# Optimization experiments

Hardware: AMD Instinct MI355X
Metric: run time of the kernel (lower is better)

Reference implementation:

```python
import jax, jax.numpy as jnp
import numpy as np

T, B, P, Q, WW, WF, C = 7, 512, 200, 64, 64, 256, 10
N = B * P
SIGMA = 0.1


def _lin(key, fin, fout):
    kw, kb = jax.random.split(key)
    s = 1.0 / np.sqrt(fin)
    return (jax.random.uniform(kw, (fin, fout), minval=-s, maxval=s),
            jax.random.uniform(kb, (fout,), minval=-s, maxval=s))


def setup_inputs() -> dict:
    key = jax.random.key(0)
    ks = jax.random.split(key, 9)
    diagms = jax.random.normal(ks[0], (T, N, 2), dtype=jnp.float32)
    # repeat_interleave(arange(B), counts): equal-sized segments of P points
    seg_ids = jnp.tile(jnp.repeat(jnp.arange(B, dtype=jnp.int32), P), (T, 1))
    theta = jax.random.normal(ks[1], (Q, 2), dtype=jnp.float32)
    w1, b1 = _lin(ks[2], 2, WW)
    w2, b2 = _lin(ks[3], WW, WW)
    w3, b3 = _lin(ks[4], WW, 1)
    r1, rb1 = _lin(ks[5], T * Q, WF)
    r2, rb2 = _lin(ks[6], WF, WF)
    r3, rb3 = _lin(ks[7], WF, C)
    return dict(diagms=diagms, seg_ids=seg_ids, theta=theta,
                w1=w1, b1=b1, w2=w2, b2=b2, w3=w3, b3=b3,
                r1=r1, rb1=rb1, r2=r2, rb2=rb2, r3=r3, rb3=rb3)


def reference(diagms, seg_ids, theta, w1, b1, w2, b2, w3, b3,
              r1, rb1, r2, rb2, r3, rb3):
    # gaussian kernel: exp(-||x - theta||^2 / (2 sigma^2)), cdist expanded
    diff = diagms[:, :, None, :] - theta[None, None, :, :]      # [T,N,Q,2]
    rep = jnp.exp(-jnp.sum(diff * diff, axis=-1) / (2.0 * SIGMA ** 2))  # [T,N,Q]
    # weight MLP on raw (birth,death) coords, shared across types
    h = jax.nn.relu(diagms @ w1 + b1)
    h = jax.nn.relu(h @ w2 + b2)
    w = jax.nn.sigmoid(h @ w3 + b3)                              # [T,N,1]
    rep = w * rep
    # global_mean_pool per diagram type via segment sum
    def pool(r, s):
        sums = jax.ops.segment_sum(r, s, num_segments=B)         # [B,Q]
        cnts = jax.ops.segment_sum(jnp.ones((r.shape[0],), r.dtype), s,
                                   num_segments=B)
        return sums / jnp.maximum(cnts, 1.0)[:, None]
    pooled = jax.vmap(pool)(rep, seg_ids)                        # [T,B,Q]
    topo = jnp.transpose(pooled, (1, 0, 2)).reshape(B, T * Q)    # cat over types
    # final MLP rho
    z = jax.nn.relu(topo @ r1 + rb1)
    z = jax.nn.relu(z @ r2 + rb2)
    return z @ r3 + rb3                                          # [B,C]
```

## Files before the change

### kernel.cpp

```cpp
#include <hip/hip_runtime.h>
#include <hip/hip_bf16.h>
#include <math.h>

#define TT 7
#define BB 512
#define PP 200
#define QQ 64
#define WWH 64
#define WF 256
#define CC 10
#define NN (BB * PP)
#define TQ (TT * QQ)

typedef __attribute__((ext_vector_type(8))) short short8;
typedef __attribute__((ext_vector_type(4))) float f32x4;

static __device__ __forceinline__ unsigned short f2bf(float f) {
    __hip_bfloat16 b = __float2bfloat16(f);
    return *reinterpret_cast<unsigned short*>(&b);
}

__global__ __launch_bounds__(256, 4) void point_weight_kernel(
    const float* __restrict__ diagms,
    const float* __restrict__ w1,
    const float* __restrict__ b1,
    const float* __restrict__ w2,
    const float* __restrict__ b2,
    const float* __restrict__ w3,
    const float* __restrict__ b3,
    float* __restrict__ w_out)
{
    __shared__ unsigned short Hl[256 * 64];
    __shared__ unsigned short W2T[64 * 64];

    const int tid  = threadIdx.x;
    const int lane = tid & 63;
    const int wv   = tid >> 6;

    {
        const int n  = tid & 63;
        const int j0 = (tid >> 6) * 16;
#pragma unroll
        for (int jj = 0; jj < 16; ++jj) {
            const int j = j0 + jj;
            const float v = w2[j * WWH + n];
            const int off = n * 64 + ((((j >> 3) ^ (n & 7))) << 3) + (j & 7);
            W2T[off] = f2bf(v);
        }
    }

    {
        const int p = tid;
        const float2 d = reinterpret_cast<const float2*>(diagms)[(size_t)blockIdx.x * 256 + p];
        const float x = d.x, y = d.y;
        uint4* Hrow = reinterpret_cast<uint4*>(Hl);
#pragma unroll
        for (int i = 0; i < 8; ++i) {
            unsigned int pk[4];
#pragma unroll
            for (int e = 0; e < 4; ++e) {
                const int j = i * 8 + 2 * e;
                const float h0 = fmaxf(fmaf(x, w1[j],     fmaf(y, w1[WWH + j],     b1[j])),     0.0f);
                const float h1 = fmaxf(fmaf(x, w1[j + 1], fmaf(y, w1[WWH + j + 1], b1[j + 1])), 0.0f);
                pk[e] = (unsigned int)f2bf(h0) | ((unsigned int)f2bf(h1) << 16);
            }
            uint4 v; v.x = pk[0]; v.y = pk[1]; v.z = pk[2]; v.w = pk[3];
            Hrow[p * 8 + (i ^ (p & 7))] = v;
        }
    }

    __syncthreads();

    float b2v[4], w3v[4];
#pragma unroll
    for (int nt = 0; nt < 4; ++nt) {
        b2v[nt] = b2[nt * 16 + (lane & 15)];
        w3v[nt] = w3[nt * 16 + (lane & 15)];
    }
    const float b3s = b3[0];

    short8 bf[2][4];
#pragma unroll
    for (int s = 0; s < 2; ++s) {
#pragma unroll
        for (int nt = 0; nt < 4; ++nt) {
            const int n = nt * 16 + (lane & 15);
            const int slot = ((lane >> 4) + s * 4) ^ (lane & 7);
            bf[s][nt] = reinterpret_cast<const short8*>(W2T)[n * 8 + slot];
        }
    }

    const int wave_p0 = wv * 64;
    const size_t out_base = (size_t)blockIdx.x * 256;

#pragma unroll 1
    for (int m = 0; m < 4; ++m) {
        f32x4 acc[4];
#pragma unroll
        for (int nt = 0; nt < 4; ++nt) acc[nt] = (f32x4){0.f, 0.f, 0.f, 0.f};

#pragma unroll
        for (int s = 0; s < 2; ++s) {
            const int p = wave_p0 + m * 16 + (lane & 15);
            const int slot = ((lane >> 4) + s * 4) ^ (lane & 7);
            const short8 af = reinterpret_cast<const short8*>(Hl)[p * 8 + slot];
#pragma unroll
            for (int nt = 0; nt < 4; ++nt) {
                acc[nt] = __builtin_amdgcn_mfma_f32_16x16x32_bf16(af, bf[s][nt], acc[nt], 0, 0, 0);
            }
        }

        float sum0 = 0.f, sum1 = 0.f, sum2 = 0.f, sum3 = 0.f;
#pragma unroll
        for (int nt = 0; nt < 4; ++nt) {
            sum0 = fmaf(fmaxf(acc[nt][0] + b2v[nt], 0.f), w3v[nt], sum0);
            sum1 = fmaf(fmaxf(acc[nt][1] + b2v[nt], 0.f), w3v[nt], sum1);
            sum2 = fmaf(fmaxf(acc[nt][2] + b2v[nt], 0.f), w3v[nt], sum2);
            sum3 = fmaf(fmaxf(acc[nt][3] + b2v[nt], 0.f), w3v[nt], sum3);
        }
#pragma unroll
        for (int off = 1; off < 16; off <<= 1) {
            sum0 += __shfl_xor(sum0, off, 64);
            sum1 += __shfl_xor(sum1, off, 64);
            sum2 += __shfl_xor(sum2, off, 64);
            sum3 += __shfl_xor(sum3, off, 64);
        }
        const int r_sel = lane & 15;
        if (r_sel < 4) {
            const float sv = (r_sel == 0) ? sum0 : (r_sel == 1) ? sum1
                           : (r_sel == 2) ? sum2 : sum3;
            const float wa = sv + b3s;
            const float wsig = 1.0f / (1.0f + __expf(-wa));
            const int prow = wave_p0 + m * 16 + ((lane >> 4) << 2) + r_sel;
            w_out[out_base + prow] = wsig;
        }
    }
}

#define NEG50_OVER_LN2 (-72.13475204444817f)

__global__ __launch_bounds__(256) void rep_pool_kernel(
    const float* __restrict__ diagms,
    const float* __restrict__ theta,
    const float* __restrict__ w_in,
    float* __restrict__ pooled)
{
    const int bid = blockIdx.x;
    const int t = bid >> 9;
    const int b = bid & (BB - 1);
    const int tid = threadIdx.x;

    __shared__ float px[PP];
    __shared__ float py[PP];
    __shared__ float wv[PP];

    if (tid < PP) {
        const int n = t * NN + b * PP + tid;
        const float2 d = reinterpret_cast<const float2*>(diagms)[n];
        px[tid] = d.x;
        py[tid] = d.y;
        wv[tid] = w_in[n];
    }
    __syncthreads();

    const int q = tid & (QQ - 1);
    const int g = tid >> 6;
    const float2 th = reinterpret_cast<const float2*>(theta)[q];
    const float tx = th.x;
    const float ty = th.y;

    float acc = 0.0f;
    const int p0 = g * (PP / 4);
#pragma unroll 5
    for (int p = p0; p < p0 + PP / 4; ++p) {
        const float dx = px[p] - tx;
        const float dy = py[p] - ty;
        acc = fmaf(wv[p], exp2f(fmaf(dx, dx, dy * dy) * NEG50_OVER_LN2), acc);
    }

    __shared__ float part[4][QQ];
    part[g][q] = acc;
    __syncthreads();

    if (tid < QQ) {
        const float s = (part[0][tid] + part[1][tid]) + (part[2][tid] + part[3][tid]);
        pooled[b * TQ + t * QQ + tid] = s * (1.0f / (float)PP);
    }
}

#define K3_ROWS 2
__global__ __launch_bounds__(256, 2) void rho_kernel(
    const float* __restrict__ pooled,
    const float* __restrict__ r1,
    const float* __restrict__ rb1,
    const float* __restrict__ r2,
    const float* __restrict__ rb2,
    const float* __restrict__ r3,
    const float* __restrict__ rb3,
    float* __restrict__ out)
{
    const int b0 = blockIdx.x * K3_ROWS;
    const int tid = threadIdx.x;

    __shared__ float tp[K3_ROWS * TQ];
    __shared__ float z1[K3_ROWS][WF];
    __shared__ float z2[K3_ROWS][WF];
    __shared__ float red[4][K3_ROWS][CC];

    {
        const float* src = pooled + (size_t)b0 * TQ;
#pragma unroll
        for (int j = 0; j < K3_ROWS * TQ; j += 256) {
            const int idx = j + tid;
            if (idx < K3_ROWS * TQ) tp[idx] = src[idx];
        }
    }
    __syncthreads();

    {
        float acc0 = rb1[tid], acc1 = rb1[tid];
        const float* r1c = r1 + tid;
        float rv0[8], rv1[8];
#pragma unroll
        for (int e = 0; e < 8; ++e) rv0[e] = r1c[e * WF];
#pragma unroll 1
        for (int i0 = 0; i0 < TQ; i0 += 16) {
#pragma unroll
            for (int e = 0; e < 8; ++e) rv1[e] = r1c[(i0 + 8 + e) * WF];
#pragma unroll
            for (int e = 0; e < 8; ++e) {
                acc0 = fmaf(tp[i0 + e],      rv0[e], acc0);
                acc1 = fmaf(tp[TQ + i0 + e], rv0[e], acc1);
            }
            if (i0 + 16 < TQ) {
#pragma unroll
                for (int e = 0; e < 8; ++e) rv0[e] = r1c[(i0 + 16 + e) * WF];
            }
#pragma unroll
            for (int e = 0; e < 8; ++e) {
                acc0 = fmaf(tp[i0 + 8 + e],      rv1[e], acc0);
                acc1 = fmaf(tp[TQ + i0 + 8 + e], rv1[e], acc1);
            }
        }
        z1[0][tid] = fmaxf(acc0, 0.0f);
        z1[1][tid] = fmaxf(acc1, 0.0f);
    }
    __syncthreads();

    {
        float acc0 = rb2[tid], acc1 = rb2[tid];
        const float* r2c = r2 + tid;
        float rv0[8], rv1[8];
#pragma unroll
        for (int e = 0; e < 8; ++e) rv0[e] = r2c[e * WF];
#pragma unroll 1
        for (int i0 = 0; i0 < WF; i0 += 16) {
#pragma unroll
            for (int e = 0; e < 8; ++e) rv1[e] = r2c[(i0 + 8 + e) * WF];
#pragma unroll
            for (int e = 0; e < 8; ++e) {
                acc0 = fmaf(z1[0][i0 + e], rv0[e], acc0);
                acc1 = fmaf(z1[1][i0 + e], rv0[e], acc1);
            }
            if (i0 + 16 < WF) {
#pragma unroll
                for (int e = 0; e < 8; ++e) rv0[e] = r2c[(i0 + 16 + e) * WF];
            }
#pragma unroll
            for (int e = 0; e < 8; ++e) {
                acc0 = fmaf(z1[0][i0 + 8 + e], rv1[e], acc0);
                acc1 = fmaf(z1[1][i0 + 8 + e], rv1[e], acc1);
            }
        }
        z2[0][tid] = fmaxf(acc0, 0.0f);
        z2[1][tid] = fmaxf(acc1, 0.0f);
    }
    __syncthreads();

    {
        const int lane = tid & 63;
        const int wvi  = tid >> 6;
        const float za = z2[0][tid];
        const float zb = z2[1][tid];
        float p0[CC], p1[CC];
#pragma unroll
        for (int c = 0; c < CC; ++c) {
            const float rc = r3[tid * CC + c];
            p0[c] = za * rc;
            p1[c] = zb * rc;
        }
#pragma unroll
        for (int off = 32; off >= 1; off >>= 1) {
#pragma unroll
            for (int c = 0; c < CC; ++c) {
                p0[c] += __shfl_xor(p0[c], off, 64);
                p1[c] += __shfl_xor(p1[c], off, 64);
            }
        }
        if (lane == 0) {
#pragma unroll
            for (int c = 0; c < CC; ++c) {
                red[wvi][0][c] = p0[c];
                red[wvi][1][c] = p1[c];
            }
        }
        __syncthreads();
        if (tid < K3_ROWS * CC) {
            const int r = tid / CC;
            const int c = tid % CC;
            out[(size_t)(b0 + r) * CC + c] =
                red[0][r][c] + red[1][r][c] + red[2][r][c] + red[3][r][c] + rb3[c];
        }
    }
}

extern "C" void kernel_launch(void* const* d_in, const int* in_sizes, int n_in,
                              void* d_out, int out_size, void* d_ws, size_t ws_size,
                              hipStream_t stream)
{
    const float* diagms = (const float*)d_in[0];
    const float* theta  = (const float*)d_in[2];
    const float* w1     = (const float*)d_in[3];
    const float* b1     = (const float*)d_in[4];
    const float* w2     = (const float*)d_in[5];
    const float* b2     = (const float*)d_in[6];
    const float* w3     = (const float*)d_in[7];
    const float* b3     = (const float*)d_in[8];
    const float* r1     = (const float*)d_in[9];
    const float* rb1    = (const float*)d_in[10];
    const float* r2     = (const float*)d_in[11];
    const float* rb2    = (const float*)d_in[12];
    const float* r3     = (const float*)d_in[13];
    const float* rb3    = (const float*)d_in[14];
    float* out = (float*)d_out;

    float* w_buf  = (float*)d_ws;
    float* pooled = w_buf + (size_t)TT * NN;

    const int total = TT * NN;

    point_weight_kernel<<<total / 256, 256, 0, stream>>>(
        diagms, w1, b1, w2, b2, w3, b3, w_buf);

    rep_pool_kernel<<<TT * BB, 256, 0, stream>>>(diagms, theta, w_buf, pooled);

    rho_kernel<<<BB / K3_ROWS, 256, 0, stream>>>(pooled, r1, rb1, r2, rb2, r3, rb3, out);
}
```

Measured before the change: 145.4 us.

## Fuse point-weight MLP into pooling kernel and split rho K-dimension across waves

Merges the per-point weight MLP kernel with the Gaussian representation pooling kernel. Each block of one diagram now computes weights for 256 loaded points, of which 200 are used, and keeps them in shared memory. This removes the global write and re-read of the weight buffer and one kernel launch, at the cost of about 28% redundant MLP work on padding points. The rho kernel now uses 1024 threads, splitting each layer's reduction dimension into four slices with a shared-memory partial sum. This adds parallelism and latency hiding to the small final MLP.

```diff
diff --git a/kernel.cpp b/kernel.cpp
--- a/kernel.cpp
+++ b/kernel.cpp
@@ -20,22 +20,32 @@
     return *reinterpret_cast<unsigned short*>(&b);
 }
 
-__global__ __launch_bounds__(256, 4) void point_weight_kernel(
+#define NEG50_OVER_LN2 (-72.13475204444817f)
+
+__global__ __launch_bounds__(256, 3) void fused_weight_pool_kernel(
     const float* __restrict__ diagms,
+    const float* __restrict__ theta,
     const float* __restrict__ w1,
     const float* __restrict__ b1,
     const float* __restrict__ w2,
     const float* __restrict__ b2,
     const float* __restrict__ w3,
     const float* __restrict__ b3,
-    float* __restrict__ w_out)
+    float* __restrict__ pooled)
 {
     __shared__ unsigned short Hl[256 * 64];
     __shared__ unsigned short W2T[64 * 64];
-
+    __shared__ float px[256];
+    __shared__ float py[256];
+    __shared__ float wv[256];
+    __shared__ float part[4][QQ];
+
+    const int bid  = blockIdx.x;
+    const int t    = bid >> 9;
+    const int b    = bid & (BB - 1);
     const int tid  = threadIdx.x;
     const int lane = tid & 63;
-    const int wv   = tid >> 6;
+    const int wvx  = tid >> 6;
 
     {
         const int n  = tid & 63;
@@ -50,9 +60,13 @@
     }
 
     {
-        const int p = tid;
-        const float2 d = reinterpret_cast<const float2*>(diagms)[(size_t)blockIdx.x * 256 + p];
+        const int base = t * NN + b * PP;
+        int gidx = base + tid;
+        if (gidx > TT * NN - 1) gidx = TT * NN - 1;
+        const float2 d = reinterpret_cast<const float2*>(diagms)[gidx];
         const float x = d.x, y = d.y;
+        px[tid] = x;
+        py[tid] = y;
         uint4* Hrow = reinterpret_cast<uint4*>(Hl);
 #pragma unroll
         for (int i = 0; i < 8; ++i) {
@@ -65,121 +79,96 @@
                 pk[e] = (unsigned int)f2bf(h0) | ((unsigned int)f2bf(h1) << 16);
             }
             uint4 v; v.x = pk[0]; v.y = pk[1]; v.z = pk[2]; v.w = pk[3];
-            Hrow[p * 8 + (i ^ (p & 7))] = v;
-        }
-    }
-
-    __syncthreads();
-
-    float b2v[4], w3v[4];
-#pragma unroll
-    for (int nt = 0; nt < 4; ++nt) {
-        b2v[nt] = b2[nt * 16 + (lane & 15)];
-        w3v[nt] = w3[nt * 16 + (lane & 15)];
-    }
-    const float b3s = b3[0];
-
-    short8 bf[2][4];
-#pragma unroll
-    for (int s = 0; s < 2; ++s) {
+            Hrow[tid * 8 + (i ^ (tid & 7))] = v;
+        }
+    }
+
+    __syncthreads();
+
+    {
+        float b2v[4], w3v[4];
 #pragma unroll
         for (int nt = 0; nt < 4; ++nt) {
-            const int n = nt * 16 + (lane & 15);
-            const int slot = ((lane >> 4) + s * 4) ^ (lane & 7);
-            bf[s][nt] = reinterpret_cast<const short8*>(W2T)[n * 8 + slot];
-        }
-    }
-
-    const int wave_p0 = wv * 64;
-    const size_t out_base = (size_t)blockIdx.x * 256;
+            b2v[nt] = b2[nt * 16 + (lane & 15)];
+            w3v[nt] = w3[nt * 16 + (lane & 15)];
+        }
+        const float b3s = b3[0];
+
+        short8 bfr[2][4];
+#pragma unroll
+        for (int s = 0; s < 2; ++s) {
+#pragma unroll
+            for (int nt = 0; nt < 4; ++nt) {
+                const int n = nt * 16 + (lane & 15);
+                const int slot = ((lane >> 4) + s * 4) ^ (lane & 7);
+                bfr[s][nt] = reinterpret_cast<const short8*>(W2T)[n * 8 + slot];
+            }
+        }
+
+        const int wave_p0 = wvx * 64;
 
 #pragma unroll 1
-    for (int m = 0; m < 4; ++m) {
-        f32x4 acc[4];
-#pragma unroll
-        for (int nt = 0; nt < 4; ++nt) acc[nt] = (f32x4){0.f, 0.f, 0.f, 0.f};
-
-#pragma unroll
-        for (int s = 0; s < 2; ++s) {
-            const int p = wave_p0 + m * 16 + (lane & 15);
-            const int slot = ((lane >> 4) + s * 4) ^ (lane & 7);
-            const short8 af = reinterpret_cast<const short8*>(Hl)[p * 8 + slot];
+        for (int m = 0; m < 4; ++m) {
+            f32x4 acc[4];
+#pragma unroll
+            for (int nt = 0; nt < 4; ++nt) acc[nt] = (f32x4){0.f, 0.f, 0.f, 0.f};
+
+#pragma unroll
+            for (int s = 0; s < 2; ++s) {
+                const int p = wave_p0 + m * 16 + (lane & 15);
+                const int slot = ((lane >> 4) + s * 4) ^ (lane & 7);
+                const short8 af = reinterpret_cast<const short8*>(Hl)[p * 8 + slot];
+#pragma unroll
+                for (int nt = 0; nt < 4; ++nt) {
+                    acc[nt] = __builtin_amdgcn_mfma_f32_16x16x32_bf16(af, bfr[s][nt], acc[nt], 0, 0, 0);
+                }
+            }
+
+            float sum0 = 0.f, sum1 = 0.f, sum2 = 0.f, sum3 = 0.f;
 #pragma unroll
             for (int nt = 0; nt < 4; ++nt) {
-                acc[nt] = __builtin_amdgcn_mfma_f32_16x16x32_bf16(af, bf[s][nt], acc[nt], 0, 0, 0);
-            }
-        }
-
-        float sum0 = 0.f, sum1 = 0.f, sum2 = 0.f, sum3 = 0.f;
-#pragma unroll
-        for (int nt = 0; nt < 4; ++nt) {
-            sum0 = fmaf(fmaxf(acc[nt][0] + b2v[nt], 0.f), w3v[nt], sum0);
-            sum1 = fmaf(fmaxf(acc[nt][1] + b2v[nt], 0.f), w3v[nt], sum1);
-            sum2 = fmaf(fmaxf(acc[nt][2] + b2v[nt], 0.f), w3v[nt], sum2);
-            sum3 = fmaf(fmaxf(acc[nt][3] + b2v[nt], 0.f), w3v[nt], sum3);
-        }
-#pragma unroll
-        for (int off = 1; off < 16; off <<= 1) {
-            sum0 += __shfl_xor(sum0, off, 64);
-            sum1 += __shfl_xor(sum1, off, 64);
-            sum2 += __shfl_xor(sum2, off, 64);
-            sum3 += __shfl_xor(sum3, off, 64);
-        }
-        const int r_sel = lane & 15;
-        if (r_sel < 4) {
-            const float sv = (r_sel == 0) ? sum0 : (r_sel == 1) ? sum1
-                           : (r_sel == 2) ? sum2 : sum3;
-            const float wa = sv + b3s;
-            const float wsig = 1.0f / (1.0f + __expf(-wa));
-            const int prow = wave_p0 + m * 16 + ((lane >> 4) << 2) + r_sel;
-            w_out[out_base + prow] = wsig;
-        }
-    }
-}
-
-#define NEG50_OVER_LN2 (-72.13475204444817f)
-
-__global__ __launch_bounds__(256) void rep_pool_kernel(
-    const float* __restrict__ diagms,
-    const float* __restrict__ theta,
-    const float* __restrict__ w_in,
-    float* __restrict__ pooled)
-{
-    const int bid = blockIdx.x;
-    const int t = bid >> 9;
-    const int b = bid & (BB - 1);
-    const int tid = threadIdx.x;
-
-    __shared__ float px[PP];
-    __shared__ float py[PP];
-    __shared__ float wv[PP];
-
-    if (tid < PP) {
-        const int n = t * NN + b * PP + tid;
-        const float2 d = reinterpret_cast<const float2*>(diagms)[n];
-        px[tid] = d.x;
-        py[tid] = d.y;
-        wv[tid] = w_in[n];
-    }
-    __syncthreads();
-
-    const int q = tid & (QQ - 1);
-    const int g = tid >> 6;
-    const float2 th = reinterpret_cast<const float2*>(theta)[q];
-    const float tx = th.x;
-    const float ty = th.y;
-
-    float acc = 0.0f;
-    const int p0 = g * (PP / 4);
+                sum0 = fmaf(fmaxf(acc[nt][0] + b2v[nt], 0.f), w3v[nt], sum0);
+                sum1 = fmaf(fmaxf(acc[nt][1] + b2v[nt], 0.f), w3v[nt], sum1);
+                sum2 = fmaf(fmaxf(acc[nt][2] + b2v[nt], 0.f), w3v[nt], sum2);
+                sum3 = fmaf(fmaxf(acc[nt][3] + b2v[nt], 0.f), w3v[nt], sum3);
+            }
+#pragma unroll
+            for (int off = 1; off < 16; off <<= 1) {
+                sum0 += __shfl_xor(sum0, off, 64);
+                sum1 += __shfl_xor(sum1, off, 64);
+                sum2 += __shfl_xor(sum2, off, 64);
+                sum3 += __shfl_xor(sum3, off, 64);
+            }
+            const int r_sel = lane & 15;
+            if (r_sel < 4) {
+                const float sv = (r_sel == 0) ? sum0 : (r_sel == 1) ? sum1
+                               : (r_sel == 2) ? sum2 : sum3;
+                const float wa = sv + b3s;
+                const int prow = wave_p0 + m * 16 + ((lane >> 4) << 2) + r_sel;
+                wv[prow] = 1.0f / (1.0f + __expf(-wa));
+            }
+        }
+    }
+
+    __syncthreads();
+
+    {
+        const int q = tid & (QQ - 1);
+        const int g = tid >> 6;
+        const float2 th = reinterpret_cast<const float2*>(theta)[q];
+        const float tx = th.x;
+        const float ty = th.y;
+
+        float acc = 0.0f;
+        const int p0 = g * (PP / 4);
 #pragma unroll 5
-    for (int p = p0; p < p0 + PP / 4; ++p) {
-        const float dx = px[p] - tx;
-        const float dy = py[p] - ty;
-        acc = fmaf(wv[p], exp2f(fmaf(dx, dx, dy * dy) * NEG50_OVER_LN2), acc);
-    }
-
-    __shared__ float part[4][QQ];
-    part[g][q] = acc;
+        for (int p = p0; p < p0 + PP / 4; ++p) {
+            const float dx = px[p] - tx;
+            const float dy = py[p] - ty;
+            acc = fmaf(wv[p], exp2f(fmaf(dx, dx, dy * dy) * NEG50_OVER_LN2), acc);
+        }
+        part[g][q] = acc;
+    }
     __syncthreads();
 
     if (tid < QQ) {
@@ -189,7 +178,7 @@
 }
 
 #define K3_ROWS 2
-__global__ __launch_bounds__(256, 2) void rho_kernel(
+__global__ __launch_bounds__(1024, 4) void rho_kernel(
     const float* __restrict__ pooled,
     const float* __restrict__ r1,
     const float* __restrict__ rb1,
@@ -199,32 +188,29 @@
     const float* __restrict__ rb3,
     float* __restrict__ out)
 {
-    const int b0 = blockIdx.x * K3_ROWS;
+    const int b0  = blockIdx.x * K3_ROWS;
     const int tid = threadIdx.x;
+    const int k   = tid & (WF - 1);
+    const int g   = tid >> 8;
 
     __shared__ float tp[K3_ROWS * TQ];
     __shared__ float z1[K3_ROWS][WF];
     __shared__ float z2[K3_ROWS][WF];
-    __shared__ float red[4][K3_ROWS][CC];
-
-    {
-        const float* src = pooled + (size_t)b0 * TQ;
-#pragma unroll
-        for (int j = 0; j < K3_ROWS * TQ; j += 256) {
-            const int idx = j + tid;
-            if (idx < K3_ROWS * TQ) tp[idx] = src[idx];
-        }
-    }
-    __syncthreads();
-
-    {
-        float acc0 = rb1[tid], acc1 = rb1[tid];
-        const float* r1c = r1 + tid;
+    __shared__ float part[4][K3_ROWS][WF];
+    __shared__ float red[8][CC];
+
+    if (tid < K3_ROWS * TQ) tp[tid] = pooled[(size_t)b0 * TQ + tid];
+    __syncthreads();
+
+    {
+        float acc0 = 0.0f, acc1 = 0.0f;
+        const float* r1c = r1 + k;
+        const int ibase = g * (TQ / 4);
         float rv0[8], rv1[8];
 #pragma unroll
-        for (int e = 0; e < 8; ++e) rv0[e] = r1c[e * WF];
+        for (int e = 0; e < 8; ++e) rv0[e] = r1c[(ibase + e) * WF];
 #pragma unroll 1
-        for (int i0 = 0; i0 < TQ; i0 += 16) {
+        for (int i0 = ibase; i0 < ibase + TQ / 4; i0 += 16) {
 #pragma unroll
             for (int e = 0; e < 8; ++e) rv1[e] = r1c[(i0 + 8 + e) * WF];
 #pragma unroll
@@ -232,7 +218,7 @@
                 acc0 = fmaf(tp[i0 + e],      rv0[e], acc0);
                 acc1 = fmaf(tp[TQ + i0 + e], rv0[e], acc1);
             }
-            if (i0 + 16 < TQ) {
+            if (i0 + 16 < ibase + TQ / 4) {
 #pragma unroll
                 for (int e = 0; e < 8; ++e) rv0[e] = r1c[(i0 + 16 + e) * WF];
             }
@@ -242,19 +228,27 @@
                 acc1 = fmaf(tp[TQ + i0 + 8 + e], rv1[e], acc1);
             }
         }
-        z1[0][tid] = fmaxf(acc0, 0.0f);
-        z1[1][tid] = fmaxf(acc1, 0.0f);
-    }
-    __syncthreads();
-
-    {
-        float acc0 = rb2[tid], acc1 = rb2[tid];
-        const float* r2c = r2 + tid;
+        part[g][0][k] = acc0;
+        part[g][1][k] = acc1;
+    }
+    __syncthreads();
+    if (tid < 2 * WF) {
+        const int r = tid >> 8;
+        const int kk = tid & (WF - 1);
+        z1[r][kk] = fmaxf(part[0][r][kk] + part[1][r][kk] +
+                          part[2][r][kk] + part[3][r][kk] + rb1[kk], 0.0f);
+    }
+    __syncthreads();
+
+    {
+        float acc0 = 0.0f, acc1 = 0.0f;
+        const float* r2c = r2 + k;
+        const int ibase = g * (WF / 4);
         float rv0[8], rv1[8];
 #pragma unroll
-        for (int e = 0; e < 8; ++e) rv0[e] = r2c[e * WF];
+        for (int e = 0; e < 8; ++e) rv0[e] = r2c[(ibase + e) * WF];
 #pragma unroll 1
-        for (int i0 = 0; i0 < WF; i0 += 16) {
+        for (int i0 = ibase; i0 < ibase + WF / 4; i0 += 16) {
 #pragma unroll
             for (int e = 0; e < 8; ++e) rv1[e] = r2c[(i0 + 8 + e) * WF];
 #pragma unroll
@@ -262,7 +256,7 @@
                 acc0 = fmaf(z1[0][i0 + e], rv0[e], acc0);
                 acc1 = fmaf(z1[1][i0 + e], rv0[e], acc1);
             }
-            if (i0 + 16 < WF) {
+            if (i0 + 16 < ibase + WF / 4) {
 #pragma unroll
                 for (int e = 0; e < 8; ++e) rv0[e] = r2c[(i0 + 16 + e) * WF];
             }
@@ -272,45 +266,44 @@
                 acc1 = fmaf(z1[1][i0 + 8 + e], rv1[e], acc1);
             }
         }
-        z2[0][tid] = fmaxf(acc0, 0.0f);
-        z2[1][tid] = fmaxf(acc1, 0.0f);
-    }
-    __syncthreads();
-
-    {
+        part[g][0][k] = acc0;
+        part[g][1][k] = acc1;
+    }
+    __syncthreads();
+    if (tid < 2 * WF) {
+        const int r = tid >> 8;
+        const int kk = tid & (WF - 1);
+        z2[r][kk] = fmaxf(part[0][r][kk] + part[1][r][kk] +
+                          part[2][r][kk] + part[3][r][kk] + rb2[kk], 0.0f);
+    }
+    __syncthreads();
+
+    if (tid < 512) {
+        const int r    = tid >> 8;
+        const int kk   = tid & (WF - 1);
         const int lane = tid & 63;
         const int wvi  = tid >> 6;
-        const float za = z2[0][tid];
-        const float zb = z2[1][tid];
-        float p0[CC], p1[CC];
-#pragma unroll
-        for (int c = 0; c < CC; ++c) {
-            const float rc = r3[tid * CC + c];
-            p0[c] = za * rc;
-            p1[c] = zb * rc;
-        }
+        const float z = z2[r][kk];
+        float p[CC];
+#pragma unroll
+        for (int c = 0; c < CC; ++c) p[c] = z * r3[kk * CC + c];
 #pragma unroll
         for (int off = 32; off >= 1; off >>= 1) {
 #pragma unroll
-            for (int c = 0; c < CC; ++c) {
-                p0[c] += __shfl_xor(p0[c], off, 64);
-                p1[c] += __shfl_xor(p1[c], off, 64);
-            }
+            for (int c = 0; c < CC; ++c) p[c] += __shfl_xor(p[c], off, 64);
         }
         if (lane == 0) {
 #pragma unroll
-            for (int c = 0; c < CC; ++c) {
-                red[wvi][0][c] = p0[c];
-                red[wvi][1][c] = p1[c];
-            }
-        }
-        __syncthreads();
-        if (tid < K3_ROWS * CC) {
-            const int r = tid / CC;
-            const int c = tid % CC;
-            out[(size_t)(b0 + r) * CC + c] =
-                red[0][r][c] + red[1][r][c] + red[2][r][c] + red[3][r][c] + rb3[c];
-        }
+            for (int c = 0; c < CC; ++c) red[wvi][c] = p[c];
+        }
+    }
+    __syncthreads();
+    if (tid < K3_ROWS * CC) {
+        const int r = tid / CC;
+        const int c = tid % CC;
+        out[(size_t)(b0 + r) * CC + c] =
+            red[r * 4 + 0][c] + red[r * 4 + 1][c] +
+            red[r * 4 + 2][c] + red[r * 4 + 3][c] + rb3[c];
     }
 }
 
@@ -334,15 +327,11 @@
     const float* rb3    = (const float*)d_in[14];
     float* out = (float*)d_out;
 
-    float* w_buf  = (float*)d_ws;
-    float* pooled = w_buf + (size_t)TT * NN;
-
-    const int total = TT * NN;
-
-    point_weight_kernel<<<total / 256, 256, 0, stream>>>(
-        diagms, w1, b1, w2, b2, w3, b3, w_buf);
-
-    rep_pool_kernel<<<TT * BB, 256, 0, stream>>>(diagms, theta, w_buf, pooled);
-
-    rho_kernel<<<BB / K3_ROWS, 256, 0, stream>>>(pooled, r1, rb1, r2, rb2, r3, rb3, out);
+    float* pooled = (float*)d_ws;
+
+    fused_weight_pool_kernel<<<TT * BB, 256, 0, stream>>>(
+        diagms, theta, w1, b1, w2, b2, w3, b3, pooled);
+
+    rho_kernel<<<BB / K3_ROWS, 1024, 0, stream>>>(
+        pooled, r1, rb1, r2, rb2, r3, rb3, out);
 }
```

Measured after the change: 135.9 us. -6.5%, faster.
